# Kernel tuning notes

Hardware: AMD Instinct MI355X
Metric: run time of the kernel (lower is better)

The kernel has to match this reference:

```python
import jax, jax.numpy as jnp
import numpy as np


def _tet_geometry(vertices, indices, tet_density):
    """Gather 4 corners per tet, compute area (|det|/6), min edge length, alpha."""
    v = vertices[indices]                      # [T,4,3]
    v0, v1, v2, v3 = v[:, 0], v[:, 1], v[:, 2], v[:, 3]
    # --- tet area: |det([v1-v0, v2-v0, v3-v0])| / 6 ---
    e1, e2, e3 = v1 - v0, v2 - v0, v3 - v0     # [T,3] each
    det = (e1[:, 0] * (e2[:, 1] * e3[:, 2] - e2[:, 2] * e3[:, 1])
           - e1[:, 1] * (e2[:, 0] * e3[:, 2] - e2[:, 2] * e3[:, 0])
           + e1[:, 2] * (e2[:, 0] * e3[:, 1] - e2[:, 1] * e3[:, 0]))
    tet_area = jnp.abs(det) / 6.0              # [T]
    # --- edge lengths of all 6 edges, take min (mode='min') ---
    edge_sq = jnp.stack([
        jnp.sum((v0 - v1) ** 2, axis=1),
        jnp.sum((v0 - v2) ** 2, axis=1),
        jnp.sum((v0 - v3) ** 2, axis=1),
        jnp.sum((v1 - v2) ** 2, axis=1),
        jnp.sum((v1 - v3) ** 2, axis=1),
        jnp.sum((v2 - v3) ** 2, axis=1),
    ], axis=0)                                 # [6,T]
    el = jnp.sqrt(jnp.min(edge_sq, axis=0))    # [T]
    tet_alpha = 1.0 - jnp.exp(-tet_density * el)
    return tet_area, tet_alpha


def _vert_density(tet_density, indices, num_verts):
    # torch scatter_reduce_ 'amax' with zero-initialized dest and include_self=True
    # == segment_max over all 4 corner slots, clamped below at 0.
    flat_idx = indices.reshape(-1)                         # [4T]
    src = jnp.repeat(tet_density, 4)                       # [4T], matches row-major flatten
    vmax = jax.ops.segment_max(src, flat_idx, num_segments=num_verts)
    return jnp.maximum(vmax, jnp.zeros((), vmax.dtype))    # untouched verts -> 0


def setup_inputs() -> dict:
    key = jax.random.key(0)
    k1, k2, k3 = jax.random.split(key, 3)
    V, T = 1_000_000, 4_000_000
    vertices = jax.random.normal(k1, (V, 3), dtype=jnp.float32)
    indices = jax.random.randint(k2, (T, 4), 0, V, dtype=jnp.int32)
    tet_density = jax.random.uniform(k3, (T,), dtype=jnp.float32)
    return {"vertices": vertices, "indices": indices, "tet_density": tet_density}


def reference(vertices, indices, tet_density):
    tet_area, tet_alpha = _tet_geometry(vertices, indices, tet_density)
    vert_density = _vert_density(tet_density, indices, vertices.shape[0])
    return tet_area, tet_alpha, vert_density
```

## Files before the change

kernel.cpp:

```cpp
#include <hip/hip_runtime.h>

typedef int nt_int4 __attribute__((ext_vector_type(4)));

#define NB     256
#define VSHIFT 12
#define BMASK  ((1 << VSHIFT) - 1)
#define BCAP   65536
#define RT     4
#define NR     4

__global__ __launch_bounds__(256) void zero_kernel(uint4* __restrict__ vd4, int n4,
                                                   unsigned* __restrict__ gcnt) {
    int i = blockIdx.x * blockDim.x + threadIdx.x;
    if (i < n4) vd4[i] = make_uint4(0u, 0u, 0u, 0u);
    if (gcnt && i < NB) gcnt[i] = 0u;
}

__global__ __launch_bounds__(256) void pad_verts_kernel(const float* __restrict__ verts,
                                                        float4* __restrict__ verts4, int V) {
    int i = blockIdx.x * blockDim.x + threadIdx.x;
    if (i < V) {
        const float* p = verts + (size_t)i * 3;
        verts4[i] = make_float4(p[0], p[1], p[2], 0.f);
    }
}

__global__ __launch_bounds__(256) void fused_geom_bin_kernel(
    const float4* __restrict__ verts4,
    const int4*  __restrict__ idx4,
    const float* __restrict__ dens,
    float* __restrict__ out_area,
    float* __restrict__ out_alpha,
    uint2*       __restrict__ pairs,
    unsigned*    __restrict__ gcnt,
    unsigned*    __restrict__ vd,
    int T)
{
    __shared__ unsigned s_cnt[NB];
    __shared__ unsigned s_run[NB];
    __shared__ unsigned s_roff[NB];
    __shared__ unsigned s_wc[NB];
    __shared__ unsigned s_scan[NB];
    __shared__ uint2    stage[256 * RT * 4];

    int tid  = threadIdx.x;
    int base = blockIdx.x * (256 * RT * NR);

    s_cnt[tid] = 0u;
    __syncthreads();
    for (int k = 0; k < RT * NR; ++k) {
        int i = base + k * 256 + tid;
        if (i < T) {
            int4 q = idx4[i];
            atomicAdd(&s_cnt[(unsigned)q.x >> VSHIFT], 1u);
            atomicAdd(&s_cnt[(unsigned)q.y >> VSHIFT], 1u);
            atomicAdd(&s_cnt[(unsigned)q.z >> VSHIFT], 1u);
            atomicAdd(&s_cnt[(unsigned)q.w >> VSHIFT], 1u);
        }
    }
    __syncthreads();

    s_run[tid] = atomicAdd(&gcnt[tid], s_cnt[tid]);
    __syncthreads();

    for (int r = 0; r < NR; ++r) {
        int4  q[RT];
        float dd[RT];
        bool  vl[RT];
#pragma unroll
        for (int k = 0; k < RT; ++k) {
            int i = base + (r * RT + k) * 256 + tid;
            vl[k] = (i < T);
            if (vl[k]) { q[k] = idx4[i]; dd[k] = dens[i]; }
        }

#pragma unroll
        for (int k = 0; k < RT; ++k) if (vl[k]) {
            int i = base + (r * RT + k) * 256 + tid;
            float4 v0 = verts4[q[k].x];
            float4 v1 = verts4[q[k].y];
            float4 v2 = verts4[q[k].z];
            float4 v3 = verts4[q[k].w];

            float e1x = v1.x - v0.x, e1y = v1.y - v0.y, e1z = v1.z - v0.z;
            float e2x = v2.x - v0.x, e2y = v2.y - v0.y, e2z = v2.z - v0.z;
            float e3x = v3.x - v0.x, e3y = v3.y - v0.y, e3z = v3.z - v0.z;

            float det = e1x * (e2y * e3z - e2z * e3y)
                      - e1y * (e2x * e3z - e2z * e3x)
                      + e1z * (e2x * e3y - e2y * e3x);
            __builtin_nontemporal_store(fabsf(det) * (1.0f / 6.0f), &out_area[i]);

            float q01 = e1x * e1x + e1y * e1y + e1z * e1z;
            float q02 = e2x * e2x + e2y * e2y + e2z * e2z;
            float q03 = e3x * e3x + e3y * e3y + e3z * e3z;
            float ax, ay, az;
            ax = v1.x - v2.x; ay = v1.y - v2.y; az = v1.z - v2.z;
            float q12 = ax * ax + ay * ay + az * az;
            ax = v1.x - v3.x; ay = v1.y - v3.y; az = v1.z - v3.z;
            float q13 = ax * ax + ay * ay + az * az;
            ax = v2.x - v3.x; ay = v2.y - v3.y; az = v2.z - v3.z;
            float q23 = ax * ax + ay * ay + az * az;

            float mn = fminf(fminf(fminf(q01, q02), fminf(q03, q12)), fminf(q13, q23));
            float el = sqrtf(mn);
            __builtin_nontemporal_store(1.0f - expf(-dd[k] * el), &out_alpha[i]);
        }

        s_cnt[tid] = 0u;
        __syncthreads();
#pragma unroll
        for (int k = 0; k < RT; ++k) if (vl[k]) {
            atomicAdd(&s_cnt[(unsigned)q[k].x >> VSHIFT], 1u);
            atomicAdd(&s_cnt[(unsigned)q[k].y >> VSHIFT], 1u);
            atomicAdd(&s_cnt[(unsigned)q[k].z >> VSHIFT], 1u);
            atomicAdd(&s_cnt[(unsigned)q[k].w >> VSHIFT], 1u);
        }
        __syncthreads();

        unsigned x = s_cnt[tid];
        s_scan[tid] = x;
        __syncthreads();
        for (int s = 1; s < NB; s <<= 1) {
            unsigned t = (tid >= s) ? s_scan[tid - s] : 0u;
            __syncthreads();
            s_scan[tid] += t;
            __syncthreads();
        }
        s_roff[tid] = s_scan[tid] - x;
        s_wc[tid]   = 0u;
        __syncthreads();
        unsigned npairs = s_scan[NB - 1];

#pragma unroll
        for (int k = 0; k < RT; ++k) if (vl[k]) {
            unsigned db = __float_as_uint(dd[k]);
            unsigned vv[4] = { (unsigned)q[k].x, (unsigned)q[k].y,
                               (unsigned)q[k].z, (unsigned)q[k].w };
#pragma unroll
            for (int j = 0; j < 4; ++j) {
                unsigned b    = vv[j] >> VSHIFT;
                unsigned slot = s_roff[b] + atomicAdd(&s_wc[b], 1u);
                stage[slot] = make_uint2(vv[j], db);
            }
        }
        __syncthreads();

        for (unsigned l = tid; l < npairs; l += 256) {
            uint2 e = stage[l];
            unsigned b  = e.x >> VSHIFT;
            unsigned rr = s_run[b] + (l - s_roff[b]);
            if (rr < BCAP) pairs[(size_t)b * BCAP + rr] = e;
            else           atomicMax(vd + e.x, e.y);
        }
        __syncthreads();

        s_run[tid] += s_cnt[tid];
        __syncthreads();
    }
}

__global__ __launch_bounds__(1024) void bucket_max_kernel(
    const uint2*    __restrict__ pairs,
    const unsigned* __restrict__ gcnt,
    unsigned*       __restrict__ vd,
    int V)
{
    __shared__ unsigned tbl[1 << VSHIFT];
    int b   = blockIdx.x;
    int tid = threadIdx.x;

    for (int j = tid; j < (1 << VSHIFT); j += 1024) tbl[j] = 0u;
    __syncthreads();

    unsigned cnt = gcnt[b];
    if (cnt > BCAP) cnt = BCAP;
    const uint2* p = pairs + (size_t)b * BCAP;
    for (unsigned i = tid; i < cnt; i += 1024) {
        uint2 e = p[i];
        atomicMax(&tbl[e.x & BMASK], e.y);
    }
    __syncthreads();

    int vbase = b << VSHIFT;
    for (int j = tid; j < (1 << VSHIFT); j += 1024) {
        int v = vbase + j;
        if (v < V) {
            unsigned cur = vd[v];
            unsigned t   = tbl[j];
            vd[v] = cur > t ? cur : t;
        }
    }
}

__global__ __launch_bounds__(256) void tet_kernel_filter(
    const float4* __restrict__ verts4,
    const int*   __restrict__ indices,
    const float* __restrict__ density,
    float* __restrict__ out_area,
    float* __restrict__ out_alpha,
    unsigned int* __restrict__ vd,
    int T)
{
    int i = blockIdx.x * blockDim.x + threadIdx.x;
    if (i >= T) return;

    nt_int4 idx = __builtin_nontemporal_load((const nt_int4*)indices + i);
    float d     = __builtin_nontemporal_load(&density[i]);
    unsigned int db = __float_as_uint(d);

    unsigned int c0 = vd[idx.x];
    unsigned int c1 = vd[idx.y];
    unsigned int c2 = vd[idx.z];
    unsigned int c3 = vd[idx.w];

    float4 v0 = verts4[idx.x];
    float4 v1 = verts4[idx.y];
    float4 v2 = verts4[idx.z];
    float4 v3 = verts4[idx.w];

    float e1x = v1.x - v0.x, e1y = v1.y - v0.y, e1z = v1.z - v0.z;
    float e2x = v2.x - v0.x, e2y = v2.y - v0.y, e2z = v2.z - v0.z;
    float e3x = v3.x - v0.x, e3y = v3.y - v0.y, e3z = v3.z - v0.z;

    float det = e1x * (e2y * e3z - e2z * e3y)
              - e1y * (e2x * e3z - e2z * e3x)
              + e1z * (e2x * e3y - e2y * e3x);
    __builtin_nontemporal_store(fabsf(det) * (1.0f / 6.0f), &out_area[i]);

    float q01 = e1x * e1x + e1y * e1y + e1z * e1z;
    float q02 = e2x * e2x + e2y * e2y + e2z * e2z;
    float q03 = e3x * e3x + e3y * e3y + e3z * e3z;
    float ax, ay, az;
    ax = v1.x - v2.x; ay = v1.y - v2.y; az = v1.z - v2.z;
    float q12 = ax * ax + ay * ay + az * az;
    ax = v1.x - v3.x; ay = v1.y - v3.y; az = v1.z - v3.z;
    float q13 = ax * ax + ay * ay + az * az;
    ax = v2.x - v3.x; ay = v2.y - v3.y; az = v2.z - v3.z;
    float q23 = ax * ax + ay * ay + az * az;

    float mn = fminf(fminf(fminf(q01, q02), fminf(q03, q12)), fminf(q13, q23));
    float el = sqrtf(mn);
    __builtin_nontemporal_store(1.0f - expf(-d * el), &out_alpha[i]);

    if (db > c0) atomicMax(vd + idx.x, db);
    if (db > c1) atomicMax(vd + idx.y, db);
    if (db > c2) atomicMax(vd + idx.z, db);
    if (db > c3) atomicMax(vd + idx.w, db);
}

__global__ __launch_bounds__(256) void tet_kernel_fb(
    const float* __restrict__ verts,
    const int4*  __restrict__ indices,
    const float* __restrict__ density,
    float* __restrict__ out_area,
    float* __restrict__ out_alpha,
    unsigned int* __restrict__ vd,
    int T)
{
    int i = blockIdx.x * blockDim.x + threadIdx.x;
    if (i >= T) return;

    int4 idx = indices[i];
    float d = density[i];

    const float* p;
    p = verts + idx.x * 3; float v0x = p[0], v0y = p[1], v0z = p[2];
    p = verts + idx.y * 3; float v1x = p[0], v1y = p[1], v1z = p[2];
    p = verts + idx.z * 3; float v2x = p[0], v2y = p[1], v2z = p[2];
    p = verts + idx.w * 3; float v3x = p[0], v3y = p[1], v3z = p[2];

    float e1x = v1x - v0x, e1y = v1y - v0y, e1z = v1z - v0z;
    float e2x = v2x - v0x, e2y = v2y - v0y, e2z = v2z - v0z;
    float e3x = v3x - v0x, e3y = v3y - v0y, e3z = v3z - v0z;

    float det = e1x * (e2y * e3z - e2z * e3y)
              - e1y * (e2x * e3z - e2z * e3x)
              + e1z * (e2x * e3y - e2y * e3x);
    out_area[i] = fabsf(det) * (1.0f / 6.0f);

    float q01 = e1x * e1x + e1y * e1y + e1z * e1z;
    float q02 = e2x * e2x + e2y * e2y + e2z * e2z;
    float q03 = e3x * e3x + e3y * e3y + e3z * e3z;
    float ax, ay, az;
    ax = v1x - v2x; ay = v1y - v2y; az = v1z - v2z;
    float q12 = ax * ax + ay * ay + az * az;
    ax = v1x - v3x; ay = v1y - v3y; az = v1z - v3z;
    float q13 = ax * ax + ay * ay + az * az;
    ax = v2x - v3x; ay = v2y - v3y; az = v2z - v3z;
    float q23 = ax * ax + ay * ay + az * az;

    float mn = fminf(fminf(fminf(q01, q02), fminf(q03, q12)), fminf(q13, q23));
    float el = sqrtf(mn);
    out_alpha[i] = 1.0f - expf(-d * el);

    unsigned int db = __float_as_uint(d);
    atomicMax(vd + idx.x, db);
    atomicMax(vd + idx.y, db);
    atomicMax(vd + idx.z, db);
    atomicMax(vd + idx.w, db);
}


extern "C" void kernel_launch(void* const* d_in, const int* in_sizes, int n_in,
                              void* d_out, int out_size, void* d_ws, size_t ws_size,
                              hipStream_t stream) {
    const float* verts   = (const float*)d_in[0];
    const int*   indices = (const int*)d_in[1];
    const float* density = (const float*)d_in[2];
    int T = in_sizes[2];
    int V = in_sizes[0] / 3;

    float* out       = (float*)d_out;
    float* out_area  = out;
    float* out_alpha = out + (size_t)T;
    unsigned int* vd = (unsigned int*)(out + 2 * (size_t)T);

    const int block = 256;
    int n4 = V / 4;

    size_t pairsB = (size_t)NB * BCAP * sizeof(uint2);
    size_t cntB   = (size_t)NB * sizeof(unsigned);
    size_t v4B    = (size_t)V * sizeof(float4);

    double mean = 4.0 * (double)T / NB;
    bool capOK = (mean + 12.0 * __builtin_sqrt(mean) <= (double)BCAP);
    bool fastOK = (V % 4 == 0) && (V <= (NB << VSHIFT)) && capOK && d_ws;

    int tetsPerBlock = block * RT * NR;
    int nbAct = (V + (1 << VSHIFT) - 1) >> VSHIFT;

    if (fastOK && ws_size >= pairsB + cntB + v4B) {
        uint2*    pairs  = (uint2*)d_ws;
        unsigned* gcnt   = (unsigned*)((char*)d_ws + pairsB);
        float4*   verts4 = (float4*)((char*)d_ws + pairsB + ((cntB + 255) & ~(size_t)255));

        zero_kernel<<<(n4 + block - 1) / block, block, 0, stream>>>((uint4*)vd, n4, gcnt);
        pad_verts_kernel<<<(V + block - 1) / block, block, 0, stream>>>(verts, verts4, V);

        fused_geom_bin_kernel<<<(T + tetsPerBlock - 1) / tetsPerBlock, block, 0, stream>>>(
            verts4, (const int4*)indices, density, out_area, out_alpha, pairs, gcnt, vd, T);

        bucket_max_kernel<<<nbAct, 1024, 0, stream>>>(pairs, gcnt, vd, V);
    } else if (d_ws && ws_size >= v4B && (V % 4) == 0) {
        zero_kernel<<<(n4 + block - 1) / block, block, 0, stream>>>((uint4*)vd, n4, nullptr);
        float4* verts4 = (float4*)d_ws;
        pad_verts_kernel<<<(V + block - 1) / block, block, 0, stream>>>(verts, verts4, V);
        tet_kernel_filter<<<(T + block - 1) / block, block, 0, stream>>>(
            verts4, indices, density, out_area, out_alpha, vd, T);
    } else {
        zero_kernel<<<(n4 + block - 1) / block, block, 0, stream>>>((uint4*)vd, n4, nullptr);
        tet_kernel_fb<<<(T + block - 1) / block, block, 0, stream>>>(
            verts, (const int4*)indices, density, out_area, out_alpha, vd, T);
    }
}
```

Baseline: 429.0 us.

## Software-pipeline vertex gathers, use wave-shuffle scan, merge setup kernels

Restructures the fused geometry/binning kernel so that the next round's index/density loads and vertex gathers are issued early and overlap with the current round's binning and scatter work. It replaces the shared-memory Hillis-Steele scan with a wavefront shuffle scan plus a cross-wave combine, removing many barriers. It also fuses the zero and vertex-padding kernels into one launch, makes the index loads nontemporal, drops a trailing barrier, and retunes RT/NR from 4x4 to 2x8. Holding prefetched vertices in registers raises register pressure and may lower occupancy.

New measurement: 438.5 us. 1.02x slower.

```diff
diff --git a/kernel.cpp b/kernel.cpp
--- a/kernel.cpp
+++ b/kernel.cpp
@@ -1,25 +1,23 @@
 #include <hip/hip_runtime.h>
 
-typedef int nt_int4 __attribute__((ext_vector_type(4)));
+typedef int          nt_int4  __attribute__((ext_vector_type(4)));
+typedef unsigned int nt_uint2 __attribute__((ext_vector_type(2)));
 
 #define NB     256
 #define VSHIFT 12
 #define BMASK  ((1 << VSHIFT) - 1)
 #define BCAP   65536
-#define RT     4
-#define NR     4
-
-__global__ __launch_bounds__(256) void zero_kernel(uint4* __restrict__ vd4, int n4,
-                                                   unsigned* __restrict__ gcnt) {
+#define RT     2
+#define NR     8
+
+__global__ __launch_bounds__(256) void setup_kernel(uint4* __restrict__ vd4, int n4,
+                                                    unsigned* __restrict__ gcnt,
+                                                    const float* __restrict__ verts,
+                                                    float4* __restrict__ verts4, int V) {
     int i = blockIdx.x * blockDim.x + threadIdx.x;
     if (i < n4) vd4[i] = make_uint4(0u, 0u, 0u, 0u);
     if (gcnt && i < NB) gcnt[i] = 0u;
-}
-
-__global__ __launch_bounds__(256) void pad_verts_kernel(const float* __restrict__ verts,
-                                                        float4* __restrict__ verts4, int V) {
-    int i = blockIdx.x * blockDim.x + threadIdx.x;
-    if (i < V) {
+    if (verts4 && i < V) {
         const float* p = verts + (size_t)i * 3;
         verts4[i] = make_float4(p[0], p[1], p[2], 0.f);
     }
@@ -40,10 +38,12 @@
     __shared__ unsigned s_run[NB];
     __shared__ unsigned s_roff[NB];
     __shared__ unsigned s_wc[NB];
-    __shared__ unsigned s_scan[NB];
+    __shared__ unsigned s_wsum[4];
     __shared__ uint2    stage[256 * RT * 4];
 
     int tid  = threadIdx.x;
+    int lane = tid & 63;
+    int wid  = tid >> 6;
     int base = blockIdx.x * (256 * RT * NR);
 
     s_cnt[tid] = 0u;
@@ -51,7 +51,7 @@
     for (int k = 0; k < RT * NR; ++k) {
         int i = base + k * 256 + tid;
         if (i < T) {
-            int4 q = idx4[i];
+            nt_int4 q = __builtin_nontemporal_load((const nt_int4*)idx4 + i);
             atomicAdd(&s_cnt[(unsigned)q.x >> VSHIFT], 1u);
             atomicAdd(&s_cnt[(unsigned)q.y >> VSHIFT], 1u);
             atomicAdd(&s_cnt[(unsigned)q.z >> VSHIFT], 1u);
@@ -63,24 +63,45 @@
     s_run[tid] = atomicAdd(&gcnt[tid], s_cnt[tid]);
     __syncthreads();
 
+    nt_int4 q[RT], qn[RT];
+    float   dd[RT], ddn[RT];
+    bool    vl[RT], vln[RT];
+    float4  pv[RT][4];
+
+#pragma unroll
+    for (int k = 0; k < RT; ++k) {
+        int i = base + k * 256 + tid;
+        vl[k] = (i < T);
+        if (vl[k]) {
+            q[k]  = __builtin_nontemporal_load((const nt_int4*)idx4 + i);
+            dd[k] = __builtin_nontemporal_load(&dens[i]);
+        }
+    }
+#pragma unroll
+    for (int k = 0; k < RT; ++k) if (vl[k]) {
+        pv[k][0] = verts4[q[k].x];
+        pv[k][1] = verts4[q[k].y];
+        pv[k][2] = verts4[q[k].z];
+        pv[k][3] = verts4[q[k].w];
+    }
+
     for (int r = 0; r < NR; ++r) {
-        int4  q[RT];
-        float dd[RT];
-        bool  vl[RT];
-#pragma unroll
-        for (int k = 0; k < RT; ++k) {
-            int i = base + (r * RT + k) * 256 + tid;
-            vl[k] = (i < T);
-            if (vl[k]) { q[k] = idx4[i]; dd[k] = dens[i]; }
+        if (r + 1 < NR) {
+#pragma unroll
+            for (int k = 0; k < RT; ++k) {
+                int i = base + ((r + 1) * RT + k) * 256 + tid;
+                vln[k] = (i < T);
+                if (vln[k]) {
+                    qn[k]  = __builtin_nontemporal_load((const nt_int4*)idx4 + i);
+                    ddn[k] = __builtin_nontemporal_load(&dens[i]);
+                }
+            }
         }
 
 #pragma unroll
         for (int k = 0; k < RT; ++k) if (vl[k]) {
             int i = base + (r * RT + k) * 256 + tid;
-            float4 v0 = verts4[q[k].x];
-            float4 v1 = verts4[q[k].y];
-            float4 v2 = verts4[q[k].z];
-            float4 v3 = verts4[q[k].w];
+            float4 v0 = pv[k][0], v1 = pv[k][1], v2 = pv[k][2], v3 = pv[k][3];
 
             float e1x = v1.x - v0.x, e1y = v1.y - v0.y, e1z = v1.z - v0.z;
             float e2x = v2.x - v0.x, e2y = v2.y - v0.y, e2z = v2.z - v0.z;
@@ -119,18 +140,31 @@
         __syncthreads();
 
         unsigned x = s_cnt[tid];
-        s_scan[tid] = x;
-        __syncthreads();
-        for (int s = 1; s < NB; s <<= 1) {
-            unsigned t = (tid >= s) ? s_scan[tid - s] : 0u;
-            __syncthreads();
-            s_scan[tid] += t;
-            __syncthreads();
-        }
-        s_roff[tid] = s_scan[tid] - x;
+        unsigned incl = x;
+#pragma unroll
+        for (int s = 1; s < 64; s <<= 1) {
+            unsigned t = __shfl_up(incl, s);
+            if (lane >= s) incl += t;
+        }
+        if (lane == 63) s_wsum[wid] = incl;
+        __syncthreads();
+        unsigned pre = 0;
+#pragma unroll
+        for (int w = 0; w < 4; ++w) pre += (w < wid) ? s_wsum[w] : 0u;
+        unsigned npairs = s_wsum[0] + s_wsum[1] + s_wsum[2] + s_wsum[3];
+        s_roff[tid] = pre + incl - x;
         s_wc[tid]   = 0u;
         __syncthreads();
-        unsigned npairs = s_scan[NB - 1];
+
+        if (r + 1 < NR) {
+#pragma unroll
+            for (int k = 0; k < RT; ++k) if (vln[k]) {
+                pv[k][0] = verts4[qn[k].x];
+                pv[k][1] = verts4[qn[k].y];
+                pv[k][2] = verts4[qn[k].z];
+                pv[k][3] = verts4[qn[k].w];
+            }
+        }
 
 #pragma unroll
         for (int k = 0; k < RT; ++k) if (vl[k]) {
@@ -156,7 +190,8 @@
         __syncthreads();
 
         s_run[tid] += s_cnt[tid];
-        __syncthreads();
+#pragma unroll
+        for (int k = 0; k < RT; ++k) { q[k] = qn[k]; dd[k] = ddn[k]; vl[k] = vln[k]; }
     }
 }
 
@@ -335,21 +370,24 @@
         unsigned* gcnt   = (unsigned*)((char*)d_ws + pairsB);
         float4*   verts4 = (float4*)((char*)d_ws + pairsB + ((cntB + 255) & ~(size_t)255));
 
-        zero_kernel<<<(n4 + block - 1) / block, block, 0, stream>>>((uint4*)vd, n4, gcnt);
-        pad_verts_kernel<<<(V + block - 1) / block, block, 0, stream>>>(verts, verts4, V);
+        int setupN = (V > n4 ? V : n4);
+        setup_kernel<<<(setupN + block - 1) / block, block, 0, stream>>>(
+            (uint4*)vd, n4, gcnt, verts, verts4, V);
 
         fused_geom_bin_kernel<<<(T + tetsPerBlock - 1) / tetsPerBlock, block, 0, stream>>>(
             verts4, (const int4*)indices, density, out_area, out_alpha, pairs, gcnt, vd, T);
 
         bucket_max_kernel<<<nbAct, 1024, 0, stream>>>(pairs, gcnt, vd, V);
     } else if (d_ws && ws_size >= v4B && (V % 4) == 0) {
-        zero_kernel<<<(n4 + block - 1) / block, block, 0, stream>>>((uint4*)vd, n4, nullptr);
         float4* verts4 = (float4*)d_ws;
-        pad_verts_kernel<<<(V + block - 1) / block, block, 0, stream>>>(verts, verts4, V);
+        int setupN = (V > n4 ? V : n4);
+        setup_kernel<<<(setupN + block - 1) / block, block, 0, stream>>>(
+            (uint4*)vd, n4, nullptr, verts, verts4, V);
         tet_kernel_filter<<<(T + block - 1) / block, block, 0, stream>>>(
             verts4, indices, density, out_area, out_alpha, vd, T);
     } else {
-        zero_kernel<<<(n4 + block - 1) / block, block, 0, stream>>>((uint4*)vd, n4, nullptr);
+        setup_kernel<<<(n4 + block - 1) / block, block, 0, stream>>>(
+            (uint4*)vd, n4, nullptr, nullptr, nullptr, 0);
         tet_kernel_fb<<<(T + block - 1) / block, block, 0, stream>>>(
             verts, (const int4*)indices, density, out_area, out_alpha, vd, T);
     }
```
